# Kernel optimization log

Hardware: AMD Instinct MI355X
Metric: run time of the kernel (lower is better)

Reference implementation:

```python
import jax, jax.numpy as jnp
import numpy as np

N = 50000
E = 640000
R = 8


def setup_inputs() -> dict:
    key = jax.random.key(0)
    ks = jax.random.split(key, 12)
    in_c, hid_c, out_c = 128, 128, 64
    s1 = 1.0 / np.sqrt(in_c)
    s2 = 1.0 / np.sqrt(hid_c)
    s3 = 1.0 / np.sqrt(out_c)
    return {
        "x": jax.random.normal(ks[0], (N, in_c), dtype=jnp.float32),
        "edge_index": jax.random.randint(ks[1], (2, E), 0, N),
        "edge_type": jax.random.randint(ks[2], (E,), 0, R),
        # layer 1: per-relation weights, root weight, bias
        "W1": jax.random.uniform(ks[3], (R, in_c, hid_c), minval=-s1, maxval=s1, dtype=jnp.float32),
        "root1": jax.random.uniform(ks[4], (in_c, hid_c), minval=-s1, maxval=s1, dtype=jnp.float32),
        "b1": jnp.zeros((hid_c,), dtype=jnp.float32),
        # layer 2
        "W2": jax.random.uniform(ks[5], (R, hid_c, out_c), minval=-s2, maxval=s2, dtype=jnp.float32),
        "root2": jax.random.uniform(ks[6], (hid_c, out_c), minval=-s2, maxval=s2, dtype=jnp.float32),
        "b2": jnp.zeros((out_c,), dtype=jnp.float32),
        # classifier
        "Wc": jax.random.uniform(ks[7], (out_c, 2), minval=-s3, maxval=s3, dtype=jnp.float32),
        "bc": jnp.zeros((2,), dtype=jnp.float32),
    }


def _rgcn_layer(x, edge_index, edge_type, W, root, b):
    # PyG RGCNConv with aggr='mean': per relation r, mean-aggregate source
    # features over edges of type r into destinations, then apply W_r.
    # out = sum_r mean_agg_r(x) @ W_r + x @ root + b
    src, dst = edge_index[0], edge_index[1]
    msgs = x[src]  # [E, Fin] gather
    seg = edge_type * N + dst  # combined (relation, dst) segment id
    sums = jax.ops.segment_sum(msgs, seg, num_segments=R * N)  # [R*N, Fin]
    cnt = jax.ops.segment_sum(jnp.ones((msgs.shape[0],), x.dtype), seg, num_segments=R * N)
    mean = sums / jnp.maximum(cnt, 1.0)[:, None]  # zero-degree -> 0
    mean = mean.reshape(R, N, x.shape[1])  # [R, N, Fin]
    out = jnp.einsum("rnf,rfo->no", mean, W) + x @ root + b
    return out


def reference(x, edge_index, edge_type, W1, root1, b1, W2, root2, b2, Wc, bc):
    h = jax.nn.relu(_rgcn_layer(x, edge_index, edge_type, W1, root1, b1))
    # dropout (p=0.3) is identity in eval mode
    h = jax.nn.relu(_rgcn_layer(h, edge_index, edge_type, W2, root2, b2))
    logits = h @ Wc + bc  # [N, 2]
    return logits
```

## Files before the change

### kernel.cpp

```cpp
#include <hip/hip_runtime.h>

#define NN 50000
#define EE 640000
#define RR 8
#define CAP 64

typedef __bf16 bf16x8 __attribute__((ext_vector_type(8)));
typedef float  f32x4  __attribute__((ext_vector_type(4)));
typedef const __attribute__((address_space(1))) unsigned int* gas_p;
typedef __attribute__((address_space(3))) unsigned int* las_p;

__device__ __forceinline__ unsigned short f2b(float f) {
  unsigned int u = __float_as_uint(f);
  u += 0x7fffu + ((u >> 16) & 1u);
  return (unsigned short)(u >> 16);
}
__device__ __forceinline__ float b2f(unsigned short h) {
  return __uint_as_float(((unsigned int)h) << 16);
}

__global__ void k_f32_to_bf16_x4(const float* __restrict__ src,
                                 unsigned short* __restrict__ dst, int n4) {
  int t = blockIdx.x * blockDim.x + threadIdx.x;
  if (t >= n4) return;
  float4 v = reinterpret_cast<const float4*>(src)[t];
  ushort4 o = make_ushort4(f2b(v.x), f2b(v.y), f2b(v.z), f2b(v.w));
  reinterpret_cast<ushort4*>(dst)[t] = o;
}

__global__ void k_build_b1(const float* __restrict__ W1, const float* __restrict__ root1,
                           unsigned short* __restrict__ B1T) {
  int t = blockIdx.x * 256 + threadIdx.x;
  if (t >= 1152 * 128) return;
  int j = t >> 7, k = t & 127;
  float v = (j < 1024) ? W1[((j >> 7) << 14) + (k << 7) + (j & 127)]
                       : root1[(k << 7) + (j - 1024)];
  B1T[t] = f2b(v);
}

__global__ void k_build_b2(const float* __restrict__ W2, const float* __restrict__ root2,
                           unsigned short* __restrict__ B2T) {
  int t = blockIdx.x * 256 + threadIdx.x;
  if (t >= 640 * 128) return;
  int j = t >> 7, k = t & 127;
  float v = 0.0f;
  if (j < 512)      v = W2[((j >> 6) << 13) + (k << 6) + (j & 63)];
  else if (j < 576) v = root2[(k << 6) + (j - 512)];
  B2T[t] = f2b(v);
}

__global__ void k_edges(const int* __restrict__ src, const int* __restrict__ dst,
                        const int* __restrict__ typ,
                        int* __restrict__ cursor, unsigned int* __restrict__ entries) {
  int e = blockIdx.x * 256 + threadIdx.x;
  if (e >= EE) return;
  int d = dst[e], r = typ[e];
  int pos = atomicAdd(&cursor[d], 1);
  if (pos < CAP)
    entries[d * CAP + pos] = (unsigned int)src[e] | ((unsigned int)r << 16);
}

__global__ __launch_bounds__(256, 2) void k_gemm(
    const unsigned short* __restrict__ A, const unsigned short* __restrict__ BT,
    unsigned short* __restrict__ Y, float* __restrict__ rootOut,
    const float* __restrict__ bias, int M, int nsplit, int nroot) {
  __shared__ __align__(16) unsigned short As[128 * 128];
  __shared__ __align__(16) unsigned short Bs[128 * 128];
  const int tid = threadIdx.x;
  const int m0 = blockIdx.x * 128;
  const int n0 = blockIdx.y * 128;
  const int wv = tid >> 6;
  const int ln = tid & 63;

  {
    unsigned short* Lbuf = (wv < 2) ? As : Bs;
    const unsigned short* Gbuf = (wv < 2) ? (A + (size_t)m0 * 128) : (BT + (size_t)n0 * 128);
    const int rbase = (wv & 1) * 64;
#pragma unroll
    for (int c = 0; c < 16; ++c) {
      int r = rbase + c * 4 + (ln >> 4);
      int c16 = ln & 15;
      int j = c16 ^ (r & 15);
      const unsigned short* gp = Gbuf + (size_t)r * 128 + j * 8;
      unsigned short* lp = Lbuf + r * 128 + c16 * 8;
      __builtin_amdgcn_global_load_lds((gas_p)(const void*)gp, (las_p)(void*)lp, 16, 0, 0);
    }
  }
  __syncthreads();

  const int lane = tid & 63;
  const int wave = tid >> 6;
  const int wm = (wave >> 1) << 6;
  const int wn = (wave & 1) << 6;
  const int l15 = lane & 15;
  const int quad = lane >> 4;
  f32x4 acc[4][4] = {};
#pragma unroll
  for (int kk = 0; kk < 4; ++kk) {
    const int sw = ((kk * 4 + quad) ^ l15) * 8;
    bf16x8 af[4], bfr[4];
#pragma unroll
    for (int i = 0; i < 4; ++i) {
      af[i]  = *reinterpret_cast<const bf16x8*>(&As[(wm + i * 16 + l15) * 128 + sw]);
      bfr[i] = *reinterpret_cast<const bf16x8*>(&Bs[(wn + i * 16 + l15) * 128 + sw]);
    }
#pragma unroll
    for (int i = 0; i < 4; ++i)
#pragma unroll
      for (int j = 0; j < 4; ++j)
        acc[i][j] = __builtin_amdgcn_mfma_f32_16x16x32_bf16(bfr[j], af[i], acc[i][j], 0, 0, 0);
  }

  if (n0 >= nsplit) {
#pragma unroll
    for (int i = 0; i < 4; ++i) {
      const int m = wm + i * 16 + l15;
      if (m0 + m >= M) continue;
#pragma unroll
      for (int j = 0; j < 4; ++j) {
        const int col = n0 + wn + j * 16 + quad * 4 - nsplit;
        if (col < nroot) {
          float4 b4 = *reinterpret_cast<const float4*>(&bias[col]);
          float4 v = make_float4(acc[i][j][0] + b4.x, acc[i][j][1] + b4.y,
                                 acc[i][j][2] + b4.z, acc[i][j][3] + b4.w);
          *reinterpret_cast<float4*>(&rootOut[(size_t)(m0 + m) * nroot + col]) = v;
        }
      }
    }
  } else {
    __syncthreads();
    unsigned short* Cs = As;
#pragma unroll
    for (int i = 0; i < 4; ++i) {
      const int m = wm + i * 16 + l15;
#pragma unroll
      for (int j = 0; j < 4; ++j) {
        const int c8 = ((wn + j * 16) >> 2) + quad;
        const int c8s = c8 ^ (l15 << 1);
        uint2 pk;
        pk.x = (unsigned int)f2b(acc[i][j][0]) | ((unsigned int)f2b(acc[i][j][1]) << 16);
        pk.y = (unsigned int)f2b(acc[i][j][2]) | ((unsigned int)f2b(acc[i][j][3]) << 16);
        *reinterpret_cast<uint2*>(&Cs[m * 128 + c8s * 4]) = pk;
      }
    }
    __syncthreads();
#pragma unroll
    for (int it = 0; it < 8; ++it) {
      const int L = tid + it * 256;
      const int m = L >> 4;
      const int c16 = L & 15;
      const int c16s = c16 ^ (m & 15);
      if (m0 + m < M) {
        uint4 v = *reinterpret_cast<const uint4*>(&Cs[m * 128 + c16s * 8]);
        *reinterpret_cast<uint4*>(&Y[(size_t)(m0 + m) * nsplit + n0 + c16 * 8]) = v;
      }
    }
  }
}

__global__ void k_agg1(const unsigned int* __restrict__ entries,
                       const int* __restrict__ cursor,
                       const unsigned short* __restrict__ y,
                       const float* __restrict__ hpre,
                       unsigned int* __restrict__ hbf) {
  const int d = blockIdx.x * 4 + (threadIdx.x >> 6);
  const int lane = threadIdx.x & 63;
  int deg = cursor[d];
  if (deg > CAP) deg = CAP;
  unsigned int e = (lane < deg) ? entries[d * CAP + lane] : 0u;
  const int myr = (e >> 16) & 7;
  float sc = 0.f;
#pragma unroll
  for (int r = 0; r < 8; ++r) {
    unsigned long long bm = __ballot(lane < deg && myr == r);
    if (myr == r) sc = __builtin_amdgcn_rcpf((float)__popcll(bm));
  }
  if (lane >= deg) sc = 0.f;
  float a0 = 0.f, a1 = 0.f, c0 = 0.f, c1 = 0.f;
  for (int i = 0; i < deg; i += 2) {
    unsigned int e0 = __shfl(e, i, 64);     float s0 = __shfl(sc, i, 64);
    unsigned int e1 = __shfl(e, i + 1, 64); float s1 = __shfl(sc, i + 1, 64);
    unsigned int pk0 = *reinterpret_cast<const unsigned int*>(
        &y[((size_t)(e0 & 0xffffu) << 10) + (((e0 >> 16) & 7u) << 7) + (lane << 1)]);
    unsigned int pk1 = *reinterpret_cast<const unsigned int*>(
        &y[((size_t)(e1 & 0xffffu) << 10) + (((e1 >> 16) & 7u) << 7) + (lane << 1)]);
    a0 += b2f((unsigned short)(pk0 & 0xffffu)) * s0;
    a1 += __uint_as_float(pk0 & 0xffff0000u) * s0;
    c0 += b2f((unsigned short)(pk1 & 0xffffu)) * s1;
    c1 += __uint_as_float(pk1 & 0xffff0000u) * s1;
  }
  a0 += c0; a1 += c1;
  float2 h = reinterpret_cast<const float2*>(hpre)[(size_t)d * 64 + lane];
  a0 = fmaxf(a0 + h.x, 0.f);
  a1 = fmaxf(a1 + h.y, 0.f);
  hbf[(size_t)d * 64 + lane] = (unsigned int)f2b(a0) | ((unsigned int)f2b(a1) << 16);
}

__global__ void k_agg2(const unsigned int* __restrict__ entries,
                       const int* __restrict__ cursor,
                       const unsigned short* __restrict__ y,
                       const float* __restrict__ hpre,
                       const float* __restrict__ Wc, const float* __restrict__ bc,
                       float* __restrict__ out) {
  const int d = blockIdx.x * 4 + (threadIdx.x >> 6);
  const int lane = threadIdx.x & 63;
  int deg = cursor[d];
  if (deg > CAP) deg = CAP;
  unsigned int e = (lane < deg) ? entries[d * CAP + lane] : 0u;
  const int myr = (e >> 16) & 7;
  float sc = 0.f;
#pragma unroll
  for (int r = 0; r < 8; ++r) {
    unsigned long long bm = __ballot(lane < deg && myr == r);
    if (myr == r) sc = __builtin_amdgcn_rcpf((float)__popcll(bm));
  }
  if (lane >= deg) sc = 0.f;
  const int half = lane >> 5;
  const int l32 = lane & 31;
  float a0 = 0.f, a1 = 0.f;
  const int T = (deg + 1) >> 1;
  for (int t = 0; t < T; ++t) {
    int i = 2 * t + half;
    unsigned int ei = __shfl(e, i, 64);
    float si = __shfl(sc, i, 64);
    unsigned int pk = *reinterpret_cast<const unsigned int*>(
        &y[((size_t)(ei & 0xffffu) << 9) + (((ei >> 16) & 7u) << 6) + (l32 << 1)]);
    a0 += b2f((unsigned short)(pk & 0xffffu)) * si;
    a1 += __uint_as_float(pk & 0xffff0000u) * si;
  }
  a0 += __shfl_xor(a0, 32, 64);
  a1 += __shfl_xor(a1, 32, 64);
  float2 h = reinterpret_cast<const float2*>(hpre)[(size_t)d * 32 + l32];
  float v0 = fmaxf(a0 + h.x, 0.f);
  float v1 = fmaxf(a1 + h.y, 0.f);
  int f0 = l32 << 1;
  float p0 = v0 * Wc[f0 * 2 + 0] + v1 * Wc[f0 * 2 + 2];
  float p1 = v0 * Wc[f0 * 2 + 1] + v1 * Wc[f0 * 2 + 3];
#pragma unroll
  for (int off = 16; off > 0; off >>= 1) {
    p0 += __shfl_down(p0, off, 64);
    p1 += __shfl_down(p1, off, 64);
  }
  if (lane == 0) {
    out[d * 2 + 0] = p0 + bc[0];
    out[d * 2 + 1] = p1 + bc[1];
  }
}

extern "C" void kernel_launch(void* const* d_in, const int* in_sizes, int n_in,
                              void* d_out, int out_size, void* d_ws, size_t ws_size,
                              hipStream_t stream) {
  const float* x     = (const float*)d_in[0];
  const int*   ei    = (const int*)d_in[1];
  const int*   et    = (const int*)d_in[2];
  const float* W1    = (const float*)d_in[3];
  const float* root1 = (const float*)d_in[4];
  const float* b1    = (const float*)d_in[5];
  const float* W2    = (const float*)d_in[6];
  const float* root2 = (const float*)d_in[7];
  const float* b2    = (const float*)d_in[8];
  const float* Wc    = (const float*)d_in[9];
  const float* bc    = (const float*)d_in[10];
  const int* srcI = ei;
  const int* dstI = ei + EE;

  char* ws = (char*)d_ws;
  unsigned short* xb      = (unsigned short*)(ws);
  unsigned int*   hbf     = (unsigned int*)(ws);
  unsigned short* B1T     = (unsigned short*)(ws + 12800000);
  unsigned short* B2T     = (unsigned short*)(ws + 13094912);
  int*            cursor  = (int*)(ws + 13258752);
  unsigned int*   entries = (unsigned int*)(ws + 13458752);
  float*          hpre    = (float*)(ws + 26258752);
  unsigned short* y1      = (unsigned short*)(ws + 51858752);
  unsigned short* y2      = y1;

  hipMemsetAsync(cursor, 0, 200000, stream);
  k_f32_to_bf16_x4<<<(1600000 + 255) / 256, 256, 0, stream>>>(x, xb, 1600000);
  k_build_b1<<<(1152 * 128 + 255) / 256, 256, 0, stream>>>(W1, root1, B1T);
  k_build_b2<<<(640 * 128 + 255) / 256, 256, 0, stream>>>(W2, root2, B2T);
  k_edges<<<(EE + 255) / 256, 256, 0, stream>>>(srcI, dstI, et, cursor, entries);

  k_gemm<<<dim3(391, 9), 256, 0, stream>>>(xb, B1T, y1, hpre, b1, NN, 1024, 128);
  k_agg1<<<NN / 4, 256, 0, stream>>>(entries, cursor, y1, hpre, hbf);

  k_gemm<<<dim3(391, 5), 256, 0, stream>>>((const unsigned short*)hbf, B2T, y2, hpre, b2, NN, 512, 64);
  k_agg2<<<NN / 4, 256, 0, stream>>>(entries, cursor, y2, hpre, Wc, bc, (float*)d_out);
}
```

Baseline: 281.5 us.

## Reorder layer-one RGCN to aggregate inputs per relation before the GEMM

Layer one now aggregates per relation before transforming, instead of transforming first. A new kernel gathers the compact bf16 input rows per edge and writes a per-node [8 relations x 128 + root] bf16 row. A K=1152 GEMM then applies all relation weights and the root weight at once, fusing bias and ReLU. This avoids writing and then randomly gathering a 1024-wide per-node projection, so the gathers hit a much smaller, cache-friendly source. The cost is a large intermediate aggregate buffer that is written and re-read, plus a serial per-edge gather loop with per-relation masked accumulation.

```diff
diff --git a/kernel.cpp b/kernel.cpp
--- a/kernel.cpp
+++ b/kernel.cpp
@@ -31,10 +31,9 @@
 __global__ void k_build_b1(const float* __restrict__ W1, const float* __restrict__ root1,
                            unsigned short* __restrict__ B1T) {
   int t = blockIdx.x * 256 + threadIdx.x;
-  if (t >= 1152 * 128) return;
-  int j = t >> 7, k = t & 127;
-  float v = (j < 1024) ? W1[((j >> 7) << 14) + (k << 7) + (j & 127)]
-                       : root1[(k << 7) + (j - 1024)];
+  int n = t / 1152, k = t - n * 1152;
+  float v = (k < 1024) ? W1[((k >> 7) << 14) + ((k & 127) << 7) + n]
+                       : root1[((k - 1024) << 7) + n];
   B1T[t] = f2b(v);
 }
 
@@ -58,6 +57,131 @@
   int pos = atomicAdd(&cursor[d], 1);
   if (pos < CAP)
     entries[d * CAP + pos] = (unsigned int)src[e] | ((unsigned int)r << 16);
+}
+
+__global__ void k_agg1x(const unsigned int* __restrict__ entries,
+                        const int* __restrict__ cursor,
+                        const unsigned int* __restrict__ x2,
+                        unsigned int* __restrict__ agg32) {
+  const int d = blockIdx.x * 4 + (threadIdx.x >> 6);
+  const int lane = threadIdx.x & 63;
+  int deg = cursor[d];
+  if (deg > CAP) deg = CAP;
+  unsigned int e = (lane < deg) ? entries[d * CAP + lane] : 0u;
+  const int myr = (e >> 16) & 7;
+  float scr[8];
+#pragma unroll
+  for (int r = 0; r < 8; ++r) {
+    unsigned long long bm = __ballot(lane < deg && myr == r);
+    int c = __popcll(bm);
+    scr[r] = (c > 0) ? __builtin_amdgcn_rcpf((float)c) : 0.f;
+  }
+  float a[8][2];
+#pragma unroll
+  for (int r = 0; r < 8; ++r) { a[r][0] = 0.f; a[r][1] = 0.f; }
+  for (int i = 0; i < deg; ++i) {
+    unsigned int ei = __shfl(e, i, 64);
+    unsigned int s = ei & 0xffffu;
+    int re = (ei >> 16) & 7;
+    unsigned int pk = x2[(size_t)s * 64 + lane];
+    float v0 = b2f((unsigned short)(pk & 0xffffu));
+    float v1 = __uint_as_float(pk & 0xffff0000u);
+#pragma unroll
+    for (int r = 0; r < 8; ++r) {
+      float msk = (re == r) ? 1.f : 0.f;
+      a[r][0] += v0 * msk;
+      a[r][1] += v1 * msk;
+    }
+  }
+#pragma unroll
+  for (int r = 0; r < 8; ++r)
+    agg32[(size_t)d * 576 + (r << 6) + lane] =
+        (unsigned int)f2b(a[r][0] * scr[r]) | ((unsigned int)f2b(a[r][1] * scr[r]) << 16);
+  agg32[(size_t)d * 576 + 512 + lane] = x2[(size_t)d * 64 + lane];
+}
+
+__global__ __launch_bounds__(256, 2) void k_gemm1(
+    const unsigned short* __restrict__ A,
+    const unsigned short* __restrict__ B1T,
+    const float* __restrict__ bias,
+    unsigned int* __restrict__ H) {
+  __shared__ __align__(16) unsigned short As[128 * 128];
+  __shared__ __align__(16) unsigned short Bs[128 * 128];
+  const int tid = threadIdx.x;
+  const int m0 = blockIdx.x * 128;
+  const int lane = tid & 63;
+  const int wave = tid >> 6;
+  const int wm = (wave >> 1) << 6;
+  const int wn = (wave & 1) << 6;
+  const int l15 = lane & 15;
+  const int quad = lane >> 4;
+  f32x4 acc[4][4] = {};
+  for (int kt = 0; kt < 9; ++kt) {
+    uint4 areg[8], breg[8];
+#pragma unroll
+    for (int i = 0; i < 8; ++i) {
+      int cix = tid + i * 256;
+      int row = cix >> 4, p = cix & 15;
+      int j = p ^ (row & 15);
+      areg[i] = *reinterpret_cast<const uint4*>(&A[(size_t)(m0 + row) * 1152 + kt * 128 + j * 8]);
+      breg[i] = *reinterpret_cast<const uint4*>(&B1T[(size_t)row * 1152 + kt * 128 + j * 8]);
+    }
+    __syncthreads();
+#pragma unroll
+    for (int i = 0; i < 8; ++i) {
+      int cix = tid + i * 256;
+      int row = cix >> 4, p = cix & 15;
+      *reinterpret_cast<uint4*>(&As[row * 128 + p * 8]) = areg[i];
+      *reinterpret_cast<uint4*>(&Bs[row * 128 + p * 8]) = breg[i];
+    }
+    __syncthreads();
+#pragma unroll
+    for (int kk = 0; kk < 4; ++kk) {
+      const int sw = ((kk * 4 + quad) ^ l15) * 8;
+      bf16x8 af[4], bfr[4];
+#pragma unroll
+      for (int i = 0; i < 4; ++i) {
+        af[i]  = *reinterpret_cast<const bf16x8*>(&As[(wm + i * 16 + l15) * 128 + sw]);
+        bfr[i] = *reinterpret_cast<const bf16x8*>(&Bs[(wn + i * 16 + l15) * 128 + sw]);
+      }
+#pragma unroll
+      for (int i = 0; i < 4; ++i)
+#pragma unroll
+        for (int j = 0; j < 4; ++j)
+          acc[i][j] = __builtin_amdgcn_mfma_f32_16x16x32_bf16(bfr[j], af[i], acc[i][j], 0, 0, 0);
+    }
+  }
+  __syncthreads();
+  unsigned short* Cs = As;
+#pragma unroll
+  for (int i = 0; i < 4; ++i) {
+    const int m = wm + i * 16 + l15;
+#pragma unroll
+    for (int j = 0; j < 4; ++j) {
+      const int col = wn + j * 16 + quad * 4;
+      float4 b4 = *reinterpret_cast<const float4*>(&bias[col]);
+      const int c8 = ((wn + j * 16) >> 2) + quad;
+      const int c8s = c8 ^ (l15 << 1);
+      uint2 pk;
+      pk.x = (unsigned int)f2b(fmaxf(acc[i][j][0] + b4.x, 0.f)) |
+             ((unsigned int)f2b(fmaxf(acc[i][j][1] + b4.y, 0.f)) << 16);
+      pk.y = (unsigned int)f2b(fmaxf(acc[i][j][2] + b4.z, 0.f)) |
+             ((unsigned int)f2b(fmaxf(acc[i][j][3] + b4.w, 0.f)) << 16);
+      *reinterpret_cast<uint2*>(&Cs[m * 128 + c8s * 4]) = pk;
+    }
+  }
+  __syncthreads();
+#pragma unroll
+  for (int it = 0; it < 8; ++it) {
+    const int L = tid + it * 256;
+    const int m = L >> 4;
+    const int c16 = L & 15;
+    const int c16s = c16 ^ (m & 15);
+    if (m0 + m < NN) {
+      uint4 v = *reinterpret_cast<const uint4*>(&Cs[m * 128 + c16s * 8]);
+      *reinterpret_cast<uint4*>(&H[(size_t)(m0 + m) * 64 + c16 * 4]) = v;
+    }
+  }
 }
 
 __global__ __launch_bounds__(256, 2) void k_gemm(
@@ -71,7 +195,6 @@
   const int n0 = blockIdx.y * 128;
   const int wv = tid >> 6;
   const int ln = tid & 63;
-
   {
     unsigned short* Lbuf = (wv < 2) ? As : Bs;
     const unsigned short* Gbuf = (wv < 2) ? (A + (size_t)m0 * 128) : (BT + (size_t)n0 * 128);
@@ -87,7 +210,6 @@
     }
   }
   __syncthreads();
-
   const int lane = tid & 63;
   const int wave = tid >> 6;
   const int wm = (wave >> 1) << 6;
@@ -110,7 +232,6 @@
       for (int j = 0; j < 4; ++j)
         acc[i][j] = __builtin_amdgcn_mfma_f32_16x16x32_bf16(bfr[j], af[i], acc[i][j], 0, 0, 0);
   }
-
   if (n0 >= nsplit) {
 #pragma unroll
     for (int i = 0; i < 4; ++i) {
@@ -158,48 +279,10 @@
   }
 }
 
-__global__ void k_agg1(const unsigned int* __restrict__ entries,
-                       const int* __restrict__ cursor,
-                       const unsigned short* __restrict__ y,
-                       const float* __restrict__ hpre,
-                       unsigned int* __restrict__ hbf) {
-  const int d = blockIdx.x * 4 + (threadIdx.x >> 6);
-  const int lane = threadIdx.x & 63;
-  int deg = cursor[d];
-  if (deg > CAP) deg = CAP;
-  unsigned int e = (lane < deg) ? entries[d * CAP + lane] : 0u;
-  const int myr = (e >> 16) & 7;
-  float sc = 0.f;
-#pragma unroll
-  for (int r = 0; r < 8; ++r) {
-    unsigned long long bm = __ballot(lane < deg && myr == r);
-    if (myr == r) sc = __builtin_amdgcn_rcpf((float)__popcll(bm));
-  }
-  if (lane >= deg) sc = 0.f;
-  float a0 = 0.f, a1 = 0.f, c0 = 0.f, c1 = 0.f;
-  for (int i = 0; i < deg; i += 2) {
-    unsigned int e0 = __shfl(e, i, 64);     float s0 = __shfl(sc, i, 64);
-    unsigned int e1 = __shfl(e, i + 1, 64); float s1 = __shfl(sc, i + 1, 64);
-    unsigned int pk0 = *reinterpret_cast<const unsigned int*>(
-        &y[((size_t)(e0 & 0xffffu) << 10) + (((e0 >> 16) & 7u) << 7) + (lane << 1)]);
-    unsigned int pk1 = *reinterpret_cast<const unsigned int*>(
-        &y[((size_t)(e1 & 0xffffu) << 10) + (((e1 >> 16) & 7u) << 7) + (lane << 1)]);
-    a0 += b2f((unsigned short)(pk0 & 0xffffu)) * s0;
-    a1 += __uint_as_float(pk0 & 0xffff0000u) * s0;
-    c0 += b2f((unsigned short)(pk1 & 0xffffu)) * s1;
-    c1 += __uint_as_float(pk1 & 0xffff0000u) * s1;
-  }
-  a0 += c0; a1 += c1;
-  float2 h = reinterpret_cast<const float2*>(hpre)[(size_t)d * 64 + lane];
-  a0 = fmaxf(a0 + h.x, 0.f);
-  a1 = fmaxf(a1 + h.y, 0.f);
-  hbf[(size_t)d * 64 + lane] = (unsigned int)f2b(a0) | ((unsigned int)f2b(a1) << 16);
-}
-
 __global__ void k_agg2(const unsigned int* __restrict__ entries,
                        const int* __restrict__ cursor,
                        const unsigned short* __restrict__ y,
-                       const float* __restrict__ hpre,
+                       const float* __restrict__ out2,
                        const float* __restrict__ Wc, const float* __restrict__ bc,
                        float* __restrict__ out) {
   const int d = blockIdx.x * 4 + (threadIdx.x >> 6);
@@ -230,9 +313,9 @@
   }
   a0 += __shfl_xor(a0, 32, 64);
   a1 += __shfl_xor(a1, 32, 64);
-  float2 h = reinterpret_cast<const float2*>(hpre)[(size_t)d * 32 + l32];
-  float v0 = fmaxf(a0 + h.x, 0.f);
-  float v1 = fmaxf(a1 + h.y, 0.f);
+  float2 h2 = reinterpret_cast<const float2*>(out2)[(size_t)d * 32 + l32];
+  float v0 = fmaxf(a0 + h2.x, 0.f);
+  float v1 = fmaxf(a1 + h2.y, 0.f);
   int f0 = l32 << 1;
   float p0 = v0 * Wc[f0 * 2 + 0] + v1 * Wc[f0 * 2 + 2];
   float p1 = v0 * Wc[f0 * 2 + 1] + v1 * Wc[f0 * 2 + 3];
@@ -266,24 +349,24 @@
 
   char* ws = (char*)d_ws;
   unsigned short* xb      = (unsigned short*)(ws);
-  unsigned int*   hbf     = (unsigned int*)(ws);
   unsigned short* B1T     = (unsigned short*)(ws + 12800000);
   unsigned short* B2T     = (unsigned short*)(ws + 13094912);
   int*            cursor  = (int*)(ws + 13258752);
   unsigned int*   entries = (unsigned int*)(ws + 13458752);
-  float*          hpre    = (float*)(ws + 26258752);
-  unsigned short* y1      = (unsigned short*)(ws + 51858752);
-  unsigned short* y2      = y1;
+  unsigned int*   hbf     = (unsigned int*)(ws + 26258752);
+  unsigned short* agg     = (unsigned short*)(ws + 39058752);
+  unsigned short* y2      = agg;
+  float*          out2    = (float*)(ws + 39058752 + 51200000);
 
   hipMemsetAsync(cursor, 0, 200000, stream);
-  k_f32_to_bf16_x4<<<(1600000 + 255) / 256, 256, 0, stream>>>(x, xb, 1600000);
-  k_build_b1<<<(1152 * 128 + 255) / 256, 256, 0, stream>>>(W1, root1, B1T);
-  k_build_b2<<<(640 * 128 + 255) / 256, 256, 0, stream>>>(W2, root2, B2T);
-  k_edges<<<(EE + 255) / 256, 256, 0, stream>>>(srcI, dstI, et, cursor, entries);
-
-  k_gemm<<<dim3(391, 9), 256, 0, stream>>>(xb, B1T, y1, hpre, b1, NN, 1024, 128);
-  k_agg1<<<NN / 4, 256, 0, stream>>>(entries, cursor, y1, hpre, hbf);
-
-  k_gemm<<<dim3(391, 5), 256, 0, stream>>>((const unsigned short*)hbf, B2T, y2, hpre, b2, NN, 512, 64);
-  k_agg2<<<NN / 4, 256, 0, stream>>>(entries, cursor, y2, hpre, Wc, bc, (float*)d_out);
-}
+  k_f32_to_bf16_x4<<<6250, 256, 0, stream>>>(x, xb, 1600000);
+  k_build_b1<<<576, 256, 0, stream>>>(W1, root1, B1T);
+  k_build_b2<<<320, 256, 0, stream>>>(W2, root2, B2T);
+  k_edges<<<2500, 256, 0, stream>>>(srcI, dstI, et, cursor, entries);
+
+  k_agg1x<<<NN / 4, 256, 0, stream>>>(entries, cursor, (const unsigned int*)xb, (unsigned int*)agg);
+  k_gemm1<<<391, 256, 0, stream>>>(agg, B1T, b1, hbf);
+
+  k_gemm<<<dim3(391, 5), 256, 0, stream>>>((const unsigned short*)hbf, B2T, y2, out2, b2, NN, 512, 64);
+  k_agg2<<<NN / 4, 256, 0, stream>>>(entries, cursor, y2, out2, Wc, bc, (float*)d_out);
+}
```

Result: slower. 365.1 us (+29.7%).

## Aggregate per-relation means before GEMM instead of transforming then gathering

Applied to the files above, without the earlier changes.

Reorders each RGCN layer. Per-relation mean aggregates of the input features are now computed first into an [N, 8*128] bf16 buffer, and a single K=1152 GEMM then applies all relation weights plus the root weight. The old order ran a wide GEMM producing per-relation outputs and gathered those. The bias, ReLU and final classifier are fused into the GEMM epilogue, which removes the fp32 hpre intermediate and the separate aggregation/classifier kernels. In exchange the per-edge gather is narrower but an extra 100 MB aggregate buffer is written and read per layer, and layer 2's K grows from 128 to 1152.

```diff
diff --git a/kernel.cpp b/kernel.cpp
--- a/kernel.cpp
+++ b/kernel.cpp
@@ -2,7 +2,6 @@
 
 #define NN 50000
 #define EE 640000
-#define RR 8
 #define CAP 64
 
 typedef __bf16 bf16x8 __attribute__((ext_vector_type(8)));
@@ -31,22 +30,21 @@
 __global__ void k_build_b1(const float* __restrict__ W1, const float* __restrict__ root1,
                            unsigned short* __restrict__ B1T) {
   int t = blockIdx.x * 256 + threadIdx.x;
-  if (t >= 1152 * 128) return;
-  int j = t >> 7, k = t & 127;
-  float v = (j < 1024) ? W1[((j >> 7) << 14) + (k << 7) + (j & 127)]
-                       : root1[(k << 7) + (j - 1024)];
+  int n = t / 1152, k = t - n * 1152;
+  float v = (k < 1024) ? W1[((k >> 7) << 14) + ((k & 127) << 7) + n]
+                       : root1[((k - 1024) << 7) + n];
   B1T[t] = f2b(v);
 }
 
-__global__ void k_build_b2(const float* __restrict__ W2, const float* __restrict__ root2,
-                           unsigned short* __restrict__ B2T) {
+__global__ void k_build_b2p(const float* __restrict__ W2, const float* __restrict__ root2,
+                            unsigned short* __restrict__ B2p) {
   int t = blockIdx.x * 256 + threadIdx.x;
-  if (t >= 640 * 128) return;
-  int j = t >> 7, k = t & 127;
-  float v = 0.0f;
-  if (j < 512)      v = W2[((j >> 6) << 13) + (k << 6) + (j & 63)];
-  else if (j < 576) v = root2[(k << 6) + (j - 512)];
-  B2T[t] = f2b(v);
+  int n = t / 1152, k = t - n * 1152;
+  float v = 0.f;
+  if (n < 64)
+    v = (k < 1024) ? W2[((k >> 7) << 13) + ((k & 127) << 6) + n]
+                   : root2[((k - 1024) << 6) + n];
+  B2p[t] = f2b(v);
 }
 
 __global__ void k_edges(const int* __restrict__ src, const int* __restrict__ dst,
@@ -60,190 +58,167 @@
     entries[d * CAP + pos] = (unsigned int)src[e] | ((unsigned int)r << 16);
 }
 
-__global__ __launch_bounds__(256, 2) void k_gemm(
-    const unsigned short* __restrict__ A, const unsigned short* __restrict__ BT,
-    unsigned short* __restrict__ Y, float* __restrict__ rootOut,
-    const float* __restrict__ bias, int M, int nsplit, int nroot) {
-  __shared__ __align__(16) unsigned short As[128 * 128];
-  __shared__ __align__(16) unsigned short Bs[128 * 128];
-  const int tid = threadIdx.x;
-  const int m0 = blockIdx.x * 128;
-  const int n0 = blockIdx.y * 128;
-  const int wv = tid >> 6;
-  const int ln = tid & 63;
-
-  {
-    unsigned short* Lbuf = (wv < 2) ? As : Bs;
-    const unsigned short* Gbuf = (wv < 2) ? (A + (size_t)m0 * 128) : (BT + (size_t)n0 * 128);
-    const int rbase = (wv & 1) * 64;
-#pragma unroll
-    for (int c = 0; c < 16; ++c) {
-      int r = rbase + c * 4 + (ln >> 4);
-      int c16 = ln & 15;
-      int j = c16 ^ (r & 15);
-      const unsigned short* gp = Gbuf + (size_t)r * 128 + j * 8;
-      unsigned short* lp = Lbuf + r * 128 + c16 * 8;
-      __builtin_amdgcn_global_load_lds((gas_p)(const void*)gp, (las_p)(void*)lp, 16, 0, 0);
-    }
-  }
-  __syncthreads();
-
-  const int lane = tid & 63;
-  const int wave = tid >> 6;
-  const int wm = (wave >> 1) << 6;
-  const int wn = (wave & 1) << 6;
-  const int l15 = lane & 15;
-  const int quad = lane >> 4;
-  f32x4 acc[4][4] = {};
-#pragma unroll
-  for (int kk = 0; kk < 4; ++kk) {
-    const int sw = ((kk * 4 + quad) ^ l15) * 8;
-    bf16x8 af[4], bfr[4];
-#pragma unroll
-    for (int i = 0; i < 4; ++i) {
-      af[i]  = *reinterpret_cast<const bf16x8*>(&As[(wm + i * 16 + l15) * 128 + sw]);
-      bfr[i] = *reinterpret_cast<const bf16x8*>(&Bs[(wn + i * 16 + l15) * 128 + sw]);
-    }
-#pragma unroll
-    for (int i = 0; i < 4; ++i)
-#pragma unroll
-      for (int j = 0; j < 4; ++j)
-        acc[i][j] = __builtin_amdgcn_mfma_f32_16x16x32_bf16(bfr[j], af[i], acc[i][j], 0, 0, 0);
-  }
-
-  if (n0 >= nsplit) {
-#pragma unroll
-    for (int i = 0; i < 4; ++i) {
-      const int m = wm + i * 16 + l15;
-      if (m0 + m >= M) continue;
-#pragma unroll
-      for (int j = 0; j < 4; ++j) {
-        const int col = n0 + wn + j * 16 + quad * 4 - nsplit;
-        if (col < nroot) {
-          float4 b4 = *reinterpret_cast<const float4*>(&bias[col]);
-          float4 v = make_float4(acc[i][j][0] + b4.x, acc[i][j][1] + b4.y,
-                                 acc[i][j][2] + b4.z, acc[i][j][3] + b4.w);
-          *reinterpret_cast<float4*>(&rootOut[(size_t)(m0 + m) * nroot + col]) = v;
-        }
-      }
-    }
-  } else {
-    __syncthreads();
-    unsigned short* Cs = As;
-#pragma unroll
-    for (int i = 0; i < 4; ++i) {
-      const int m = wm + i * 16 + l15;
-#pragma unroll
-      for (int j = 0; j < 4; ++j) {
-        const int c8 = ((wn + j * 16) >> 2) + quad;
-        const int c8s = c8 ^ (l15 << 1);
-        uint2 pk;
-        pk.x = (unsigned int)f2b(acc[i][j][0]) | ((unsigned int)f2b(acc[i][j][1]) << 16);
-        pk.y = (unsigned int)f2b(acc[i][j][2]) | ((unsigned int)f2b(acc[i][j][3]) << 16);
-        *reinterpret_cast<uint2*>(&Cs[m * 128 + c8s * 4]) = pk;
-      }
-    }
-    __syncthreads();
-#pragma unroll
-    for (int it = 0; it < 8; ++it) {
-      const int L = tid + it * 256;
-      const int m = L >> 4;
-      const int c16 = L & 15;
-      const int c16s = c16 ^ (m & 15);
-      if (m0 + m < M) {
-        uint4 v = *reinterpret_cast<const uint4*>(&Cs[m * 128 + c16s * 8]);
-        *reinterpret_cast<uint4*>(&Y[(size_t)(m0 + m) * nsplit + n0 + c16 * 8]) = v;
-      }
-    }
-  }
-}
-
-__global__ void k_agg1(const unsigned int* __restrict__ entries,
+__global__ void k_aggx(const unsigned int* __restrict__ entries,
                        const int* __restrict__ cursor,
-                       const unsigned short* __restrict__ y,
-                       const float* __restrict__ hpre,
-                       unsigned int* __restrict__ hbf) {
+                       const unsigned int* __restrict__ src2,
+                       unsigned int* __restrict__ agg32) {
   const int d = blockIdx.x * 4 + (threadIdx.x >> 6);
   const int lane = threadIdx.x & 63;
   int deg = cursor[d];
   if (deg > CAP) deg = CAP;
   unsigned int e = (lane < deg) ? entries[d * CAP + lane] : 0u;
   const int myr = (e >> 16) & 7;
-  float sc = 0.f;
+  float scr[8];
 #pragma unroll
   for (int r = 0; r < 8; ++r) {
     unsigned long long bm = __ballot(lane < deg && myr == r);
-    if (myr == r) sc = __builtin_amdgcn_rcpf((float)__popcll(bm));
-  }
-  if (lane >= deg) sc = 0.f;
-  float a0 = 0.f, a1 = 0.f, c0 = 0.f, c1 = 0.f;
-  for (int i = 0; i < deg; i += 2) {
-    unsigned int e0 = __shfl(e, i, 64);     float s0 = __shfl(sc, i, 64);
-    unsigned int e1 = __shfl(e, i + 1, 64); float s1 = __shfl(sc, i + 1, 64);
-    unsigned int pk0 = *reinterpret_cast<const unsigned int*>(
-        &y[((size_t)(e0 & 0xffffu) << 10) + (((e0 >> 16) & 7u) << 7) + (lane << 1)]);
-    unsigned int pk1 = *reinterpret_cast<const unsigned int*>(
-        &y[((size_t)(e1 & 0xffffu) << 10) + (((e1 >> 16) & 7u) << 7) + (lane << 1)]);
-    a0 += b2f((unsigned short)(pk0 & 0xffffu)) * s0;
-    a1 += __uint_as_float(pk0 & 0xffff0000u) * s0;
-    c0 += b2f((unsigned short)(pk1 & 0xffffu)) * s1;
-    c1 += __uint_as_float(pk1 & 0xffff0000u) * s1;
-  }
-  a0 += c0; a1 += c1;
-  float2 h = reinterpret_cast<const float2*>(hpre)[(size_t)d * 64 + lane];
-  a0 = fmaxf(a0 + h.x, 0.f);
-  a1 = fmaxf(a1 + h.y, 0.f);
-  hbf[(size_t)d * 64 + lane] = (unsigned int)f2b(a0) | ((unsigned int)f2b(a1) << 16);
-}
-
-__global__ void k_agg2(const unsigned int* __restrict__ entries,
-                       const int* __restrict__ cursor,
-                       const unsigned short* __restrict__ y,
-                       const float* __restrict__ hpre,
-                       const float* __restrict__ Wc, const float* __restrict__ bc,
-                       float* __restrict__ out) {
-  const int d = blockIdx.x * 4 + (threadIdx.x >> 6);
-  const int lane = threadIdx.x & 63;
-  int deg = cursor[d];
-  if (deg > CAP) deg = CAP;
-  unsigned int e = (lane < deg) ? entries[d * CAP + lane] : 0u;
-  const int myr = (e >> 16) & 7;
-  float sc = 0.f;
-#pragma unroll
-  for (int r = 0; r < 8; ++r) {
-    unsigned long long bm = __ballot(lane < deg && myr == r);
-    if (myr == r) sc = __builtin_amdgcn_rcpf((float)__popcll(bm));
-  }
-  if (lane >= deg) sc = 0.f;
-  const int half = lane >> 5;
-  const int l32 = lane & 31;
-  float a0 = 0.f, a1 = 0.f;
-  const int T = (deg + 1) >> 1;
-  for (int t = 0; t < T; ++t) {
-    int i = 2 * t + half;
+    int c = __popcll(bm);
+    scr[r] = (c > 0) ? __builtin_amdgcn_rcpf((float)c) : 0.f;
+  }
+  float a[8][2];
+#pragma unroll
+  for (int r = 0; r < 8; ++r) { a[r][0] = 0.f; a[r][1] = 0.f; }
+  for (int i = 0; i < deg; ++i) {
     unsigned int ei = __shfl(e, i, 64);
-    float si = __shfl(sc, i, 64);
-    unsigned int pk = *reinterpret_cast<const unsigned int*>(
-        &y[((size_t)(ei & 0xffffu) << 9) + (((ei >> 16) & 7u) << 6) + (l32 << 1)]);
-    a0 += b2f((unsigned short)(pk & 0xffffu)) * si;
-    a1 += __uint_as_float(pk & 0xffff0000u) * si;
-  }
-  a0 += __shfl_xor(a0, 32, 64);
-  a1 += __shfl_xor(a1, 32, 64);
-  float2 h = reinterpret_cast<const float2*>(hpre)[(size_t)d * 32 + l32];
-  float v0 = fmaxf(a0 + h.x, 0.f);
-  float v1 = fmaxf(a1 + h.y, 0.f);
-  int f0 = l32 << 1;
-  float p0 = v0 * Wc[f0 * 2 + 0] + v1 * Wc[f0 * 2 + 2];
-  float p1 = v0 * Wc[f0 * 2 + 1] + v1 * Wc[f0 * 2 + 3];
-#pragma unroll
-  for (int off = 16; off > 0; off >>= 1) {
-    p0 += __shfl_down(p0, off, 64);
-    p1 += __shfl_down(p1, off, 64);
-  }
-  if (lane == 0) {
-    out[d * 2 + 0] = p0 + bc[0];
-    out[d * 2 + 1] = p1 + bc[1];
+    unsigned int s = ei & 0xffffu;
+    int re = (ei >> 16) & 7;
+    unsigned int pk = src2[(size_t)s * 64 + lane];
+    float v0 = b2f((unsigned short)(pk & 0xffffu));
+    float v1 = __uint_as_float(pk & 0xffff0000u);
+#pragma unroll
+    for (int r = 0; r < 8; ++r) {
+      float msk = (re == r) ? 1.f : 0.f;
+      a[r][0] += v0 * msk;
+      a[r][1] += v1 * msk;
+    }
+  }
+#pragma unroll
+  for (int r = 0; r < 8; ++r)
+    agg32[(size_t)d * 512 + (r << 6) + lane] =
+        (unsigned int)f2b(a[r][0] * scr[r]) | ((unsigned int)f2b(a[r][1] * scr[r]) << 16);
+}
+
+__global__ __launch_bounds__(256, 3) void k_gemm_agg(
+    const unsigned int* __restrict__ Ag,
+    const unsigned int* __restrict__ X2,
+    const unsigned short* __restrict__ BT,
+    const float* __restrict__ bias,
+    unsigned int* __restrict__ H,
+    const float* __restrict__ b2,
+    const float* __restrict__ Wc,
+    const float* __restrict__ bc,
+    float* __restrict__ out,
+    int mode) {
+  __shared__ __align__(16) unsigned short Asb[64 * 128];
+  __shared__ __align__(16) unsigned short Bs[128 * 128];
+  const int tid = threadIdx.x;
+  const int m0 = blockIdx.x * 64;
+  const int lane = tid & 63;
+  const int w = tid >> 6;
+  const int l15 = lane & 15;
+  const int quad = lane >> 4;
+  const int wm = (w & 1) * 32;
+  const int wn = (w >> 1) * 64;
+  f32x4 acc[2][4] = {};
+  for (int kt = 0; kt < 9; ++kt) {
+#pragma unroll
+    for (int c = 0; c < 8; ++c) {
+      int r = w * 32 + c * 4 + (lane >> 4);
+      int c16 = lane & 15;
+      int j = c16 ^ (r & 15);
+      const unsigned short* gp = BT + (size_t)r * 1152 + kt * 128 + j * 8;
+      unsigned short* lp = Bs + r * 128 + c16 * 8;
+      __builtin_amdgcn_global_load_lds((gas_p)(const void*)gp, (las_p)(void*)lp, 16, 0, 0);
+    }
+#pragma unroll
+    for (int c = 0; c < 4; ++c) {
+      int cix = tid + c * 256;
+      int row = cix >> 4, p = cix & 15;
+      int j = p ^ (row & 15);
+      uint4 v = make_uint4(0u, 0u, 0u, 0u);
+      if (m0 + row < NN) {
+        const unsigned int* bp = (kt < 8) ? (Ag + (size_t)(m0 + row) * 512 + kt * 64)
+                                          : (X2 + (size_t)(m0 + row) * 64);
+        v = *reinterpret_cast<const uint4*>(bp + j * 4);
+      }
+      *reinterpret_cast<uint4*>(&Asb[row * 128 + p * 8]) = v;
+    }
+    __syncthreads();
+#pragma unroll
+    for (int kk = 0; kk < 4; ++kk) {
+      const int sw = ((kk * 4 + quad) ^ l15) * 8;
+      bf16x8 af[2], bfr[4];
+#pragma unroll
+      for (int i = 0; i < 2; ++i)
+        af[i] = *reinterpret_cast<const bf16x8*>(&Asb[(wm + i * 16 + l15) * 128 + sw]);
+#pragma unroll
+      for (int j = 0; j < 4; ++j)
+        bfr[j] = *reinterpret_cast<const bf16x8*>(&Bs[(wn + j * 16 + l15) * 128 + sw]);
+#pragma unroll
+      for (int i = 0; i < 2; ++i)
+#pragma unroll
+        for (int j = 0; j < 4; ++j)
+          acc[i][j] = __builtin_amdgcn_mfma_f32_16x16x32_bf16(bfr[j], af[i], acc[i][j], 0, 0, 0);
+    }
+    __syncthreads();
+  }
+  if (mode == 0) {
+    unsigned short* Cs = Asb;
+#pragma unroll
+    for (int i = 0; i < 2; ++i) {
+      const int m = wm + i * 16 + l15;
+#pragma unroll
+      for (int j = 0; j < 4; ++j) {
+        const int col = wn + j * 16 + quad * 4;
+        float4 b4 = *reinterpret_cast<const float4*>(&bias[col]);
+        const int c8 = ((wn + j * 16) >> 2) + quad;
+        const int c8s = c8 ^ (l15 << 1);
+        uint2 pk;
+        pk.x = (unsigned int)f2b(fmaxf(acc[i][j][0] + b4.x, 0.f)) |
+               ((unsigned int)f2b(fmaxf(acc[i][j][1] + b4.y, 0.f)) << 16);
+        pk.y = (unsigned int)f2b(fmaxf(acc[i][j][2] + b4.z, 0.f)) |
+               ((unsigned int)f2b(fmaxf(acc[i][j][3] + b4.w, 0.f)) << 16);
+        *reinterpret_cast<uint2*>(&Cs[m * 128 + c8s * 4]) = pk;
+      }
+    }
+    __syncthreads();
+#pragma unroll
+    for (int it = 0; it < 4; ++it) {
+      const int L = tid + it * 256;
+      const int m = L >> 4;
+      const int c16 = L & 15;
+      const int c16s = c16 ^ (m & 15);
+      if (m0 + m < NN) {
+        uint4 v = *reinterpret_cast<const uint4*>(&Cs[m * 128 + c16s * 8]);
+        *reinterpret_cast<uint4*>(&H[(size_t)(m0 + m) * 64 + c16 * 4]) = v;
+      }
+    }
+  } else {
+    if (wn == 0) {
+      const float2* wc2 = reinterpret_cast<const float2*>(Wc);
+#pragma unroll
+      for (int i = 0; i < 2; ++i) {
+        const int m = wm + i * 16 + l15;
+        float p0 = 0.f, p1 = 0.f;
+#pragma unroll
+        for (int j = 0; j < 4; ++j) {
+#pragma unroll
+          for (int rg = 0; rg < 4; ++rg) {
+            int col = j * 16 + quad * 4 + rg;
+            float v = fmaxf(acc[i][j][rg] + b2[col], 0.f);
+            float2 wv = wc2[col];
+            p0 += v * wv.x;
+            p1 += v * wv.y;
+          }
+        }
+        p0 += __shfl_xor(p0, 16, 64); p0 += __shfl_xor(p0, 32, 64);
+        p1 += __shfl_xor(p1, 16, 64); p1 += __shfl_xor(p1, 32, 64);
+        if (quad == 0 && m0 + m < NN) {
+          out[(size_t)(m0 + m) * 2 + 0] = p0 + bc[0];
+          out[(size_t)(m0 + m) * 2 + 1] = p1 + bc[1];
+        }
+      }
+    }
   }
 }
 
@@ -265,25 +240,25 @@
   const int* dstI = ei + EE;
 
   char* ws = (char*)d_ws;
-  unsigned short* xb      = (unsigned short*)(ws);
-  unsigned int*   hbf     = (unsigned int*)(ws);
+  unsigned int*   xb      = (unsigned int*)(ws);
   unsigned short* B1T     = (unsigned short*)(ws + 12800000);
-  unsigned short* B2T     = (unsigned short*)(ws + 13094912);
-  int*            cursor  = (int*)(ws + 13258752);
-  unsigned int*   entries = (unsigned int*)(ws + 13458752);
-  float*          hpre    = (float*)(ws + 26258752);
-  unsigned short* y1      = (unsigned short*)(ws + 51858752);
-  unsigned short* y2      = y1;
+  unsigned short* B2p     = (unsigned short*)(ws + 13094912);
+  int*            cursor  = (int*)(ws + 13389824);
+  unsigned int*   entries = (unsigned int*)(ws + 13589824);
+  unsigned int*   hbf     = (unsigned int*)(ws + 26389824);
+  unsigned int*   agg     = (unsigned int*)(ws + 39189824);
 
   hipMemsetAsync(cursor, 0, 200000, stream);
-  k_f32_to_bf16_x4<<<(1600000 + 255) / 256, 256, 0, stream>>>(x, xb, 1600000);
-  k_build_b1<<<(1152 * 128 + 255) / 256, 256, 0, stream>>>(W1, root1, B1T);
-  k_build_b2<<<(640 * 128 + 255) / 256, 256, 0, stream>>>(W2, root2, B2T);
-  k_edges<<<(EE + 255) / 256, 256, 0, stream>>>(srcI, dstI, et, cursor, entries);
-
-  k_gemm<<<dim3(391, 9), 256, 0, stream>>>(xb, B1T, y1, hpre, b1, NN, 1024, 128);
-  k_agg1<<<NN / 4, 256, 0, stream>>>(entries, cursor, y1, hpre, hbf);
-
-  k_gemm<<<dim3(391, 5), 256, 0, stream>>>((const unsigned short*)hbf, B2T, y2, hpre, b2, NN, 512, 64);
-  k_agg2<<<NN / 4, 256, 0, stream>>>(entries, cursor, y2, hpre, Wc, bc, (float*)d_out);
-}
+  k_f32_to_bf16_x4<<<6250, 256, 0, stream>>>(x, (unsigned short*)xb, 1600000);
+  k_build_b1<<<576, 256, 0, stream>>>(W1, root1, B1T);
+  k_build_b2p<<<576, 256, 0, stream>>>(W2, root2, B2p);
+  k_edges<<<2500, 256, 0, stream>>>(srcI, dstI, et, cursor, entries);
+
+  k_aggx<<<NN / 4, 256, 0, stream>>>(entries, cursor, xb, agg);
+  k_gemm_agg<<<(NN + 63) / 64, 256, 0, stream>>>(agg, xb, B1T, b1, hbf,
+                                                 b2, Wc, bc, (float*)d_out, 0);
+
+  k_aggx<<<NN / 4, 256, 0, stream>>>(entries, cursor, hbf, agg);
+  k_gemm_agg<<<(NN + 63) / 64, 256, 0, stream>>>(agg, hbf, B2p, b1, hbf,
+                                                 b2, Wc, bc, (float*)d_out, 1);
+}
```

Measured after the change: 346.9 us. 23.2% more time.
